# Kernel optimization log

Hardware: AMD Instinct MI355X
Metric: run time of the kernel (lower is better)

Reference implementation:

```python
import jax, jax.numpy as jnp
import numpy as np

# Hyperparameters (from init_kwargs)
D_MODEL = 1024
D_STATE = 64
HEADDIM = 64
MIMO_RANK = 2
CHUNK = 128
EXPAND = 2
D_INNER = EXPAND * D_MODEL            # 2048
NHEADS = D_INNER // HEADDIM           # 32
G = MIMO_RANK * D_STATE               # effective state channels per head = 128
D_CONV = 4
D_XBC = D_INNER + 2 * NHEADS * G      # conv channels
D_IN_PROJ = 2 * D_INNER + 2 * NHEADS * G + NHEADS  # [z, x, B, C, dt]


def rmsnorm(x, w, eps=1e-5):
    return x * w * jax.lax.rsqrt(jnp.mean(x * x, axis=-1, keepdims=True) + eps)


def setup_inputs() -> dict:
    key = jax.random.key(0)
    ks = jax.random.split(key, 8)
    B, L = 2, 2048
    x = jax.random.normal(ks[0], (B, L, D_MODEL), jnp.float32)
    norm_w = jnp.ones((D_MODEL,), jnp.float32)
    in_proj_w = jax.random.normal(ks[1], (D_IN_PROJ, D_MODEL), jnp.float32) * 0.02
    conv_w = jax.random.normal(ks[2], (D_XBC, D_CONV), jnp.float32) * 0.2
    conv_b = jnp.zeros((D_XBC,), jnp.float32)
    dt_bias = jax.random.uniform(ks[3], (NHEADS,), jnp.float32, minval=-4.0, maxval=-1.0)
    A_log = jnp.log(jax.random.uniform(ks[4], (NHEADS,), jnp.float32, minval=1.0, maxval=8.0))
    D_skip = jnp.ones((NHEADS,), jnp.float32)
    gnorm_w = jnp.ones((D_INNER,), jnp.float32)
    out_proj_w = jax.random.normal(ks[5], (D_MODEL, D_INNER), jnp.float32) * 0.02
    return dict(x=x, norm_w=norm_w, in_proj_w=in_proj_w, conv_w=conv_w, conv_b=conv_b,
                dt_bias=dt_bias, A_log=A_log, D_skip=D_skip, gnorm_w=gnorm_w,
                out_proj_w=out_proj_w)


def _mamba3(u, in_proj_w, conv_w, conv_b, dt_bias, A_log, D_skip, gnorm_w, out_proj_w):
    B, L, _ = u.shape
    H, P = NHEADS, HEADDIM
    nc = L // CHUNK

    zxbcdt = u @ in_proj_w.T                                   # (B,L,D_IN_PROJ)
    z, xbc, dt_raw = jnp.split(zxbcdt, [D_INNER, D_INNER + D_XBC], axis=-1)

    # causal depthwise conv (width D_CONV) + SiLU on [x, B, C]
    xp = jnp.pad(xbc, ((0, 0), (D_CONV - 1, 0), (0, 0)))
    conv = conv_b + sum(xp[:, k:k + L, :] * conv_w[:, k] for k in range(D_CONV))
    xbc = jax.nn.silu(conv)
    xh, Bm, Cm = jnp.split(xbc, [D_INNER, D_INNER + H * G], axis=-1)

    Xc = xh.reshape(B, nc, CHUNK, H, P)
    Bc = Bm.reshape(B, nc, CHUNK, H, G)
    Cc = Cm.reshape(B, nc, CHUNK, H, G)

    dt = jax.nn.softplus(dt_raw + dt_bias)                     # (B,L,H), positive
    A = -jnp.exp(A_log)                                        # (H,), negative
    dtc = dt.reshape(B, nc, CHUNK, H)
    a = dtc * A                                                # log decay, (B,nc,cs,H)
    cum = jnp.cumsum(a, axis=2)                                # inclusive cumsum within chunk

    # intra-chunk (quadratic, causal) part
    cumT = cum.transpose(0, 1, 3, 2)                           # (B,nc,H,cs)
    diff = cumT[..., :, None] - cumT[..., None, :]             # cum_l - cum_s
    mask = jnp.tril(jnp.ones((CHUNK, CHUNK), bool))
    decay = jnp.where(mask, jnp.exp(jnp.where(mask, diff, 0.0)), 0.0)
    dtT = dtc.transpose(0, 1, 3, 2)                            # (B,nc,H,cs)
    scores = jnp.einsum('bclhg,bcshg->bchls', Cc, Bc) * decay * dtT[:, :, :, None, :]
    Y_intra = jnp.einsum('bchls,bcshp->bclhp', scores, Xc)

    # inter-chunk state recurrence
    w = jnp.exp(cum[:, :, -1:, :] - cum) * dtc                 # (B,nc,cs,H)
    S = jnp.einsum('bcshg,bcshp->bchgp', Bc * w[..., None], Xc)  # chunk states
    dlast = jnp.exp(cum[:, :, -1, :])                          # (B,nc,H) total chunk decay

    def step(carry, inp):
        dl, s = inp
        return dl[:, :, None, None] * carry + s, carry

    init = jnp.zeros((B, H, G, P), u.dtype)
    _, Hprev = jax.lax.scan(step, init, (dlast.transpose(1, 0, 2), S.transpose(1, 0, 2, 3, 4)))
    Hprev = Hprev.transpose(1, 0, 2, 3, 4)                     # (B,nc,H,G,P) state before chunk
    Y_inter = jnp.einsum('bclhg,bchgp->bclhp', Cc * jnp.exp(cum)[..., None], Hprev)

    y = (Y_intra + Y_inter + D_skip[:, None] * Xc).reshape(B, L, D_INNER)
    y = rmsnorm(y * jax.nn.silu(z), gnorm_w)                   # gated RMSNorm
    return y @ out_proj_w.T


def reference(x, norm_w, in_proj_w, conv_w, conv_b, dt_bias, A_log, D_skip, gnorm_w, out_proj_w):
    # pre-norm residual wrapper
    return x + _mamba3(rmsnorm(x, norm_w), in_proj_w, conv_w, conv_b,
                       dt_bias, A_log, D_skip, gnorm_w, out_proj_w)
```

## Files before the change

### kernel.cpp

```cpp
#include <hip/hip_runtime.h>

typedef unsigned short u16;
typedef __attribute__((ext_vector_type(8))) short bf16x8;
typedef __attribute__((ext_vector_type(4))) float f32x4;

#define MFMA16(a,b,c) __builtin_amdgcn_mfma_f32_16x16x32_bf16(a,b,c,0,0,0)

#define DMODEL   1024
#define DINNER   2048
#define NHEADS   32
#define HEADDIM  64
#define GDIM     128
#define DXBC     10240
#define DPROJ    12320
#define CHUNK_L  128
#define NCHUNK   16
#define NROWS    4096

__device__ __forceinline__ float b2f(u16 u){ return __uint_as_float(((unsigned)u)<<16); }
__device__ __forceinline__ u16 f2b(float f){
  unsigned u = __float_as_uint(f);
  u += 0x7fffu + ((u>>16)&1u);
  return (u16)(u>>16);
}

__device__ __forceinline__ void gload_lds16(const void* g, void* l){
  __builtin_amdgcn_global_load_lds(
      (const __attribute__((address_space(1))) unsigned int*)g,
      (__attribute__((address_space(3))) unsigned int*)l, 16, 0, 0);
}

__global__ void k_f32_to_bf16(const float* __restrict__ src, u16* __restrict__ dst, int n){
  int i = blockIdx.x*blockDim.x + threadIdx.x;
  int stride = gridDim.x*blockDim.x;
  int n4 = n >> 2;
  for (int j=i; j<n4; j+=stride){
    float4 v = reinterpret_cast<const float4*>(src)[j];
    uint2 o;
    o.x = (unsigned)f2b(v.x) | ((unsigned)f2b(v.y)<<16);
    o.y = (unsigned)f2b(v.z) | ((unsigned)f2b(v.w)<<16);
    reinterpret_cast<uint2*>(dst)[j] = o;
  }
}

__global__ __launch_bounds__(256) void k_rmsnorm_in(const float* __restrict__ x,
                                                    const float* __restrict__ w,
                                                    u16* __restrict__ u){
  int row = blockIdx.x, tid = threadIdx.x;
  float4 v = reinterpret_cast<const float4*>(x + (size_t)row*DMODEL)[tid];
  float ss = v.x*v.x + v.y*v.y + v.z*v.z + v.w*v.w;
  #pragma unroll
  for (int off=32; off>0; off>>=1) ss += __shfl_down(ss, off, 64);
  __shared__ float red[4];
  if ((tid&63)==0) red[tid>>6] = ss;
  __syncthreads();
  float tot = red[0]+red[1]+red[2]+red[3];
  float sc = rsqrtf(tot/(float)DMODEL + 1e-5f);
  float4 wv = reinterpret_cast<const float4*>(w)[tid];
  uint2 o;
  o.x = (unsigned)f2b(v.x*wv.x*sc) | ((unsigned)f2b(v.y*wv.y*sc)<<16);
  o.y = (unsigned)f2b(v.z*wv.z*sc) | ((unsigned)f2b(v.w*wv.w*sc)<<16);
  reinterpret_cast<uint2*>(u + (size_t)row*DMODEL)[tid] = o;
}

__global__ __launch_bounds__(512) void k_gemm1_8p(const u16* __restrict__ A,
                                                  const u16* __restrict__ W,
                                                  u16* __restrict__ zb,
                                                  u16* __restrict__ xbc){
  __shared__ __align__(16) u16 lds[65536];
  const int tid  = threadIdx.x;
  const int lane = tid & 63, w = tid >> 6;
  const int wr = w >> 2, wc = w & 3;
  int bid = blockIdx.x;
  int xcd = bid & 7, g = bid >> 3;
  int st  = xcd*6 + (g >> 4);
  int wi  = g & 15;
  int tm  = (st/12)*4 + (wi>>2);
  int tn  = (st%12)*4 + (wi&3);
  const int m0 = tm*256, n0 = tn*256;

  const int srow = w*8 + (lane>>3);
  const int scol = ((lane&7) ^ ((lane>>3)&7))*8;
  const u16* aS = A + (size_t)(m0 + srow)*DMODEL + scol;
  const u16* bS = W + (size_t)(n0 + srow)*DMODEL + scol;
  const int ldsw = w*512;

  const int rr = lane & 15, gq = lane >> 4;

  f32x4 acc[8][4];
  #pragma unroll
  for (int i=0;i<8;i++)
    #pragma unroll
    for (int j=0;j<4;j++) acc[i][j] = (f32x4){0,0,0,0};

  auto SU_A = [&](int kt, int j){
    gload_lds16(aS + (size_t)(j*64)*DMODEL + kt*64,
                lds + (kt&1)*32768 + j*4096 + ldsw);
  };
  auto SU_B = [&](int kt, int j){
    gload_lds16(bS + (size_t)(j*64)*DMODEL + kt*64,
                lds + (kt&1)*32768 + 16384 + j*4096 + ldsw);
  };

  SU_A(0,0); SU_A(0,2); SU_B(0,0); SU_B(0,2); SU_B(0,1); SU_B(0,3); SU_A(0,1); SU_A(0,3);
  asm volatile("s_waitcnt vmcnt(2)" ::: "memory");
  __builtin_amdgcn_s_barrier();
  __builtin_amdgcn_sched_barrier(0);

  for (int kt = 0; kt < 16; ++kt){
    const u16* bufA = lds + (kt&1)*32768;
    const u16* bufB = bufA + 16384;
    const bool stg = (kt < 15);
    bf16x8 af[4][2], bw0[2][2], bw1[2][2];

    auto RDA = [&](int ti, int ks)->bf16x8{
      int r = wr*128 + ti*16 + rr;
      int s = (ks*4 + gq) ^ (rr & 7);
      return *(const bf16x8*)&bufA[r*64 + s*8];
    };
    auto RDB = [&](int tj, int ks)->bf16x8{
      int r = wc*64 + tj*16 + rr;
      int s = (ks*4 + gq) ^ (rr & 7);
      return *(const bf16x8*)&bufB[r*64 + s*8];
    };

    #pragma unroll
    for (int ti=0;ti<4;ti++){ af[ti][0]=RDA(ti,0); af[ti][1]=RDA(ti,1); }
    #pragma unroll
    for (int tj=0;tj<2;tj++){ bw0[tj][0]=RDB(tj,0); bw0[tj][1]=RDB(tj,1); }
    if (stg){ SU_A(kt+1,0); SU_A(kt+1,2); }
    __builtin_amdgcn_s_barrier();
    asm volatile("s_waitcnt lgkmcnt(0)" ::: "memory");
    __builtin_amdgcn_sched_barrier(0);
    __builtin_amdgcn_s_setprio(1);
    #pragma unroll
    for (int ti=0;ti<4;ti++)
      #pragma unroll
      for (int tj=0;tj<2;tj++){
        acc[ti][tj] = MFMA16(af[ti][0], bw0[tj][0], acc[ti][tj]);
        acc[ti][tj] = MFMA16(af[ti][1], bw0[tj][1], acc[ti][tj]);
      }
    __builtin_amdgcn_s_setprio(0);
    __builtin_amdgcn_s_barrier();

    #pragma unroll
    for (int tj=0;tj<2;tj++){ bw1[tj][0]=RDB(tj+2,0); bw1[tj][1]=RDB(tj+2,1); }
    if (stg){ SU_B(kt+1,0); SU_B(kt+1,2); }
    __builtin_amdgcn_s_barrier();
    asm volatile("s_waitcnt lgkmcnt(0)" ::: "memory");
    __builtin_amdgcn_sched_barrier(0);
    __builtin_amdgcn_s_setprio(1);
    #pragma unroll
    for (int ti=0;ti<4;ti++)
      #pragma unroll
      for (int tj=0;tj<2;tj++){
        acc[ti][tj+2] = MFMA16(af[ti][0], bw1[tj][0], acc[ti][tj+2]);
        acc[ti][tj+2] = MFMA16(af[ti][1], bw1[tj][1], acc[ti][tj+2]);
      }
    __builtin_amdgcn_s_setprio(0);
    if (stg) asm volatile("s_waitcnt vmcnt(4)" ::: "memory");
    else     asm volatile("s_waitcnt vmcnt(0)" ::: "memory");
    __builtin_amdgcn_s_barrier();

    #pragma unroll
    for (int ti=0;ti<4;ti++){ af[ti][0]=RDA(ti+4,0); af[ti][1]=RDA(ti+4,1); }
    if (stg){ SU_B(kt+1,1); SU_B(kt+1,3); }
    __builtin_amdgcn_s_barrier();
    asm volatile("s_waitcnt lgkmcnt(0)" ::: "memory");
    __builtin_amdgcn_sched_barrier(0);
    __builtin_amdgcn_s_setprio(1);
    #pragma unroll
    for (int ti=0;ti<4;ti++)
      #pragma unroll
      for (int tj=0;tj<2;tj++){
        acc[4+ti][tj] = MFMA16(af[ti][0], bw0[tj][0], acc[4+ti][tj]);
        acc[4+ti][tj] = MFMA16(af[ti][1], bw0[tj][1], acc[4+ti][tj]);
      }
    __builtin_amdgcn_s_setprio(0);
    __builtin_amdgcn_s_barrier();

    if (stg){ SU_A(kt+1,1); SU_A(kt+1,3); }
    __builtin_amdgcn_s_barrier();
    __builtin_amdgcn_sched_barrier(0);
    __builtin_amdgcn_s_setprio(1);
    #pragma unroll
    for (int ti=0;ti<4;ti++)
      #pragma unroll
      for (int tj=0;tj<2;tj++){
        acc[4+ti][tj+2] = MFMA16(af[ti][0], bw1[tj][0], acc[4+ti][tj+2]);
        acc[4+ti][tj+2] = MFMA16(af[ti][1], bw1[tj][1], acc[4+ti][tj+2]);
      }
    __builtin_amdgcn_s_setprio(0);
    if (stg){
      asm volatile("s_waitcnt vmcnt(2)" ::: "memory");
      __builtin_amdgcn_s_barrier();
      __builtin_amdgcn_sched_barrier(0);
    }
  }

  const int row0 = m0 + wr*128 + (lane>>4)*4;
  const int colb = wc*64 + (lane&15);
  if (tn >= 8){
    const int cb = n0 - DINNER;
    #pragma unroll
    for (int ti=0;ti<8;ti++)
      #pragma unroll
      for (int tj=0;tj<4;tj++)
        #pragma unroll
        for (int q=0;q<4;q++)
          xbc[(size_t)(row0 + ti*16 + q)*DXBC + cb + colb + tj*16] = f2b(acc[ti][tj][q]);
  } else {
    #pragma unroll
    for (int ti=0;ti<8;ti++)
      #pragma unroll
      for (int tj=0;tj<4;tj++)
        #pragma unroll
        for (int q=0;q<4;q++)
          zb[(size_t)(row0 + ti*16 + q)*DINNER + n0 + colb + tj*16] = f2b(acc[ti][tj][q]);
  }
}

__global__ __launch_bounds__(256) void k_gemm_dt(const u16* __restrict__ A,
                                                 const u16* __restrict__ W,
                                                 float* __restrict__ dtraw){
  const int lane = threadIdx.x & 63, wv = threadIdx.x >> 6;
  const int m0 = blockIdx.x*32;
  const int n0 = DINNER + DXBC;
  const int r  = lane & 15;
  const int kb = (lane>>4)*8;
  const int k0 = wv*256;
  const u16* a0p = A + (size_t)(m0 + r)*DMODEL + k0 + kb;
  const u16* a1p = a0p + 16*DMODEL;
  const u16* b0p = W + (size_t)(n0 + r)*DMODEL + k0 + kb;
  const u16* b1p = b0p + 16*DMODEL;
  f32x4 acc00={0,0,0,0}, acc01={0,0,0,0}, acc10={0,0,0,0}, acc11={0,0,0,0};
  #pragma unroll
  for (int k=0;k<256;k+=32){
    bf16x8 a0 = *(const bf16x8*)(a0p + k);
    bf16x8 a1 = *(const bf16x8*)(a1p + k);
    bf16x8 b0 = *(const bf16x8*)(b0p + k);
    bf16x8 b1 = *(const bf16x8*)(b1p + k);
    acc00 = MFMA16(a0,b0,acc00);
    acc01 = MFMA16(a0,b1,acc01);
    acc10 = MFMA16(a1,b0,acc10);
    acc11 = MFMA16(a1,b1,acc11);
  }
  __shared__ float part[4][1024];
  int rowb = (lane>>4)*4, col = lane&15;
  #pragma unroll
  for (int rr=0; rr<4; rr++){
    part[wv][(rowb+rr)*32 + col]         = acc00[rr];
    part[wv][(rowb+rr)*32 + col+16]      = acc01[rr];
    part[wv][(rowb+16+rr)*32 + col]      = acc10[rr];
    part[wv][(rowb+16+rr)*32 + col+16]   = acc11[rr];
  }
  __syncthreads();
  int idx = threadIdx.x*4;
  #pragma unroll
  for (int q=0;q<4;q++){
    int i = idx+q;
    dtraw[(size_t)m0*NHEADS + i] = part[0][i]+part[1][i]+part[2][i]+part[3][i];
  }
}

__global__ __launch_bounds__(256) void k_conv(const u16* __restrict__ xbc,
                                              const float* __restrict__ cw,
                                              const float* __restrict__ cb,
                                              u16* __restrict__ xh,
                                              u16* __restrict__ Bm,
                                              u16* __restrict__ Cm){
  int c  = (blockIdx.x*256 + threadIdx.x)*2;
  int row0 = blockIdx.y*8;
  int l0 = row0 & 2047;
  float4 wa = reinterpret_cast<const float4*>(cw)[c];
  float4 wb = reinterpret_cast<const float4*>(cw)[c+1];
  float cba = cb[c], cbb = cb[c+1];
  float a3=0,a2=0,a1=0, b3=0,b2=0,b1=0;
  auto loadpair = [&](int rw, float& fa, float& fb){
    unsigned v = *(const unsigned*)&xbc[(size_t)rw*DXBC + c];
    fa = b2f((u16)v); fb = b2f((u16)(v>>16));
  };
  if (l0 >= 3){
    loadpair(row0-3, a3,b3); loadpair(row0-2, a2,b2); loadpair(row0-1, a1,b1);
  }
  #pragma unroll
  for (int i=0;i<8;i++){
    float a0,b0; loadpair(row0+i, a0,b0);
    float sa = cba + a3*wa.x + a2*wa.y + a1*wa.z + a0*wa.w;
    float sb = cbb + b3*wb.x + b2*wb.y + b1*wb.z + b0*wb.w;
    sa = sa/(1.f+expf(-sa)); sb = sb/(1.f+expf(-sb));
    unsigned o = (unsigned)f2b(sa) | ((unsigned)f2b(sb)<<16);
    int rw = row0 + i;
    if (c < DINNER)            *(unsigned*)&xh[(size_t)rw*DINNER + c] = o;
    else if (c < DINNER+4096)  *(unsigned*)&Bm[(size_t)rw*4096 + (c-DINNER)] = o;
    else                       *(unsigned*)&Cm[(size_t)rw*4096 + (c-DINNER-4096)] = o;
    a3=a2; a2=a1; a1=a0; b3=b2; b2=b1; b1=b0;
  }
}

__global__ __launch_bounds__(128) void k_dtscan(const float* __restrict__ dtraw,
                                                const float* __restrict__ dt_bias,
                                                const float* __restrict__ A_log,
                                                float* __restrict__ dtT,
                                                float* __restrict__ cumT){
  int blk = blockIdx.x;
  int h   = blk & 31;
  int bc  = blk >> 5;
  int s   = threadIdx.x;
  int row = bc*128 + s;
  float xv = dtraw[(size_t)row*NHEADS + h] + dt_bias[h];
  float dt = (xv > 20.f) ? xv : log1pf(expf(xv));
  float a  = dt * (-expf(A_log[h]));
  __shared__ float lds[128];
  lds[s] = a; __syncthreads();
  #pragma unroll
  for (int off=1; off<128; off<<=1){
    float t = (s>=off) ? lds[s-off] : 0.f;
    __syncthreads();
    lds[s] += t;
    __syncthreads();
  }
  dtT[(size_t)blk*128 + s]  = dt;
  cumT[(size_t)blk*128 + s] = lds[s];
}

__global__ __launch_bounds__(256) void k_states(const u16* __restrict__ Bm,
                                                const u16* __restrict__ xh,
                                                const float* __restrict__ dtT,
                                                const float* __restrict__ cumT,
                                                float* __restrict__ S){
  int blk = blockIdx.x;
  int h = blk & 31, bc = blk >> 5;
  __shared__ __align__(16) u16 Bw[128][136];
  __shared__ __align__(16) u16 XT[64][136];
  __shared__ float cum[128], dtv[128];
  int tid = threadIdx.x;
  if (tid < 128){ cum[tid] = cumT[(size_t)blk*128+tid]; dtv[tid] = dtT[(size_t)blk*128+tid]; }
  __syncthreads();
  float clast = cum[127];
  for (int i = tid; i < 128*128; i += 256){
    int s = i >> 7, g = i & 127;
    float w = expf(clast - cum[s]) * dtv[s];
    Bw[g][s] = f2b(b2f(Bm[(size_t)(bc*128+s)*4096 + h*128 + g]) * w);
  }
  for (int i = tid; i < 64*128; i += 256){
    int s = i >> 6, p = i & 63;
    XT[p][s] = xh[(size_t)(bc*128+s)*DINNER + h*64 + p];
  }
  __syncthreads();
  int lane = tid & 63, wv = tid >> 6;
  int r = lane & 15, kb = (lane>>4)*8;
  f32x4 acc[2][4];
  #pragma unroll
  for (int i=0;i<2;i++)
    #pragma unroll
    for (int j=0;j<4;j++) acc[i][j] = (f32x4){0,0,0,0};
  #pragma unroll
  for (int k=0;k<128;k+=32){
    bf16x8 a0 = *(const bf16x8*)&Bw[wv*32 + r][k+kb];
    bf16x8 a1 = *(const bf16x8*)&Bw[wv*32 + 16 + r][k+kb];
    #pragma unroll
    for (int tj=0;tj<4;tj++){
      bf16x8 bb = *(const bf16x8*)&XT[tj*16 + r][k+kb];
      acc[0][tj] = MFMA16(a0,bb,acc[0][tj]);
      acc[1][tj] = MFMA16(a1,bb,acc[1][tj]);
    }
  }
  float* Sp = S + (size_t)blk*8192;
  int g0 = wv*32 + (lane>>4)*4, p0 = lane&15;
  #pragma unroll
  for (int ti=0;ti<2;ti++)
    #pragma unroll
    for (int tj=0;tj<4;tj++)
      #pragma unroll
      for (int rr=0;rr<4;rr++)
        Sp[(g0 + ti*16 + rr)*64 + tj*16 + p0] = acc[ti][tj][rr];
}

__global__ __launch_bounds__(256) void k_scan(const float* __restrict__ S,
                                              const float* __restrict__ cumT,
                                              u16* __restrict__ Hp){
  int slice = blockIdx.x & 7;
  int bh = blockIdx.x >> 3;
  int b = bh >> 5, h = bh & 31;
  int e0 = slice*1024 + threadIdx.x*4;
  float4 carry = {0,0,0,0};
  for (int c=0;c<NCHUNK;c++){
    int blk = (b*16+c)*32 + h;
    float dl = expf(cumT[(size_t)blk*128 + 127]);
    float4 s = *(const float4*)&S[(size_t)blk*8192 + e0];
    uint2 o;
    o.x = (unsigned)f2b(carry.x) | ((unsigned)f2b(carry.y)<<16);
    o.y = (unsigned)f2b(carry.z) | ((unsigned)f2b(carry.w)<<16);
    *reinterpret_cast<uint2*>(&Hp[(size_t)blk*8192 + e0]) = o;
    carry.x = dl*carry.x + s.x;
    carry.y = dl*carry.y + s.y;
    carry.z = dl*carry.z + s.z;
    carry.w = dl*carry.w + s.w;
  }
}

__global__ __launch_bounds__(256) void k_intra(const u16* __restrict__ Cm,
                                               const u16* __restrict__ Bm,
                                               const u16* __restrict__ xh,
                                               const u16* __restrict__ Hp,
                                               const float* __restrict__ dtT,
                                               const float* __restrict__ cumT,
                                               const float* __restrict__ Dskip,
                                               u16* __restrict__ yh){
  int blk = blockIdx.x;
  int h = blk & 31, bc = blk >> 5;
  __shared__ __align__(16) u16 Cl[128][136];
  __shared__ __align__(16) u16 Bl[128][136];
  __shared__ __align__(16) u16 XT[64][136];
  __shared__ __align__(16) u16 HT[64][136];
  __shared__ float cum[128], dtv[128];
  int tid = threadIdx.x;
  if (tid < 128){ cum[tid] = cumT[(size_t)blk*128+tid]; dtv[tid] = dtT[(size_t)blk*128+tid]; }
  for (int i = tid; i < 128*128; i += 256){
    int rw = i >> 7, g = i & 127;
    Cl[rw][g] = Cm[(size_t)(bc*128+rw)*4096 + h*128 + g];
    Bl[rw][g] = Bm[(size_t)(bc*128+rw)*4096 + h*128 + g];
  }
  for (int i = tid; i < 64*128; i += 256){
    int s = i >> 6, p = i & 63;
    XT[p][s] = xh[(size_t)(bc*128+s)*DINNER + h*64 + p];
  }
  for (int i = tid; i < 64*128; i += 256){
    int g = i >> 6, p = i & 63;
    HT[p][g] = Hp[(size_t)blk*8192 + g*64 + p];
  }
  __syncthreads();
  int lane = tid & 63, wv = tid >> 6;
  int r = lane & 15, kb = (lane>>4)*8;

  f32x4 p1[2][8];
  #pragma unroll
  for (int i=0;i<2;i++)
    #pragma unroll
    for (int j=0;j<8;j++) p1[i][j] = (f32x4){0,0,0,0};
  #pragma unroll
  for (int k=0;k<128;k+=32){
    bf16x8 a0 = *(const bf16x8*)&Cl[wv*32 + r][k+kb];
    bf16x8 a1 = *(const bf16x8*)&Cl[wv*32 + 16 + r][k+kb];
    #pragma unroll
    for (int tj=0;tj<8;tj++){
      bf16x8 bb = *(const bf16x8*)&Bl[tj*16 + r][k+kb];
      p1[0][tj] = MFMA16(a0,bb,p1[0][tj]);
      p1[1][tj] = MFMA16(a1,bb,p1[1][tj]);
    }
  }
  __syncthreads();
  int row0 = wv*32 + (lane>>4)*4;
  #pragma unroll
  for (int ti=0;ti<2;ti++)
    #pragma unroll
    for (int tj=0;tj<8;tj++)
      #pragma unroll
      for (int rr=0;rr<4;rr++){
        int l = row0 + ti*16 + rr;
        int s = tj*16 + (lane&15);
        float v = p1[ti][tj][rr];
        v = (s <= l) ? v * expf(cum[l]-cum[s]) * dtv[s] : 0.f;
        Bl[l][s] = f2b(v);
      }
  __syncthreads();

  f32x4 y[2][4];
  #pragma unroll
  for (int i=0;i<2;i++)
    #pragma unroll
    for (int j=0;j<4;j++) y[i][j] = (f32x4){0,0,0,0};
  #pragma unroll
  for (int k=0;k<128;k+=32){
    bf16x8 a0 = *(const bf16x8*)&Cl[wv*32 + r][k+kb];
    bf16x8 a1 = *(const bf16x8*)&Cl[wv*32 + 16 + r][k+kb];
    #pragma unroll
    for (int tj=0;tj<4;tj++){
      bf16x8 bb = *(const bf16x8*)&HT[tj*16 + r][k+kb];
      y[0][tj] = MFMA16(a0,bb,y[0][tj]);
      y[1][tj] = MFMA16(a1,bb,y[1][tj]);
    }
  }
  #pragma unroll
  for (int ti=0;ti<2;ti++){
    #pragma unroll
    for (int rr=0;rr<4;rr++){
      float e = expf(cum[row0 + ti*16 + rr]);
      #pragma unroll
      for (int tj=0;tj<4;tj++) y[ti][tj][rr] *= e;
    }
  }
  #pragma unroll
  for (int k=0;k<128;k+=32){
    bf16x8 a0 = *(const bf16x8*)&Bl[wv*32 + r][k+kb];
    bf16x8 a1 = *(const bf16x8*)&Bl[wv*32 + 16 + r][k+kb];
    #pragma unroll
    for (int tj=0;tj<4;tj++){
      bf16x8 bb = *(const bf16x8*)&XT[tj*16 + r][k+kb];
      y[0][tj] = MFMA16(a0,bb,y[0][tj]);
      y[1][tj] = MFMA16(a1,bb,y[1][tj]);
    }
  }
  float Dh = Dskip[h];
  #pragma unroll
  for (int ti=0;ti<2;ti++)
    #pragma unroll
    for (int tj=0;tj<4;tj++)
      #pragma unroll
      for (int rr=0;rr<4;rr++){
        int l = row0 + ti*16 + rr;
        int p = tj*16 + (lane&15);
        float xv = b2f(XT[p][l]);
        yh[(size_t)(bc*128 + l)*DINNER + h*64 + p] = f2b(y[ti][tj][rr] + Dh*xv);
      }
}

__global__ __launch_bounds__(256) void k_gate(const u16* __restrict__ yh,
                                              const u16* __restrict__ zb,
                                              const float* __restrict__ gw,
                                              u16* __restrict__ out){
  int row = blockIdx.x, tid = threadIdx.x;
  const uint4 yv = reinterpret_cast<const uint4*>(yh + (size_t)row*DINNER)[tid];
  const uint4 zv = reinterpret_cast<const uint4*>(zb + (size_t)row*DINNER)[tid];
  const unsigned* yp = (const unsigned*)&yv;
  const unsigned* zp = (const unsigned*)&zv;
  float t[8]; float ss = 0.f;
  #pragma unroll
  for (int i=0;i<4;i++){
    float y0 = b2f((u16)yp[i]), y1 = b2f((u16)(yp[i]>>16));
    float z0 = b2f((u16)zp[i]), z1 = b2f((u16)(zp[i]>>16));
    float v0 = y0 * (z0 / (1.f + expf(-z0)));
    float v1 = y1 * (z1 / (1.f + expf(-z1)));
    t[2*i] = v0; t[2*i+1] = v1; ss += v0*v0 + v1*v1;
  }
  #pragma unroll
  for (int off=32; off>0; off>>=1) ss += __shfl_down(ss, off, 64);
  __shared__ float red[4];
  if ((tid&63)==0) red[tid>>6] = ss;
  __syncthreads();
  float tot = red[0]+red[1]+red[2]+red[3];
  float g = rsqrtf(tot/(float)DINNER + 1e-5f);
  const float4 g0 = reinterpret_cast<const float4*>(gw)[tid*2];
  const float4 g1 = reinterpret_cast<const float4*>(gw)[tid*2+1];
  uint4 o;
  unsigned* op = (unsigned*)&o;
  float gg[8] = {g0.x,g0.y,g0.z,g0.w,g1.x,g1.y,g1.z,g1.w};
  #pragma unroll
  for (int i=0;i<4;i++)
    op[i] = (unsigned)f2b(t[2*i]*gg[2*i]*g) | ((unsigned)f2b(t[2*i+1]*gg[2*i+1]*g)<<16);
  reinterpret_cast<uint4*>(out + (size_t)row*DINNER)[tid] = o;
}

__global__ __launch_bounds__(256) void k_gemm2_db(const u16* __restrict__ A,
                                                  const u16* __restrict__ W,
                                                  const float* __restrict__ xres,
                                                  float* __restrict__ out){
  __shared__ __align__(16) u16 lds[2*8192];
  const int tid  = threadIdx.x;
  const int lane = tid & 63, wv = tid >> 6;
  const int wr = wv >> 1, wc = wv & 1;
  const int NWG = 8*32, Q = NWG/8;
  int swz = (blockIdx.x & 7)*Q + (blockIdx.x >> 3);
  int tm = swz / 8, tn = swz % 8;
  int m0 = tm*128, n0 = tn*128;

  const int K = DINNER;
  const int srcslot = ((lane&3) ^ ((lane>>3)&3)) * 8;
  const u16* aS0 = A + (size_t)(m0 + wv*32 + (lane>>2))*K + srcslot;
  const u16* aS1 = aS0 + (size_t)16*K;
  const u16* bS0 = W + (size_t)(n0 + wv*32 + (lane>>2))*K + srcslot;
  const u16* bS1 = bS0 + (size_t)16*K;
  const int ldsW = (wv*32)*32;
  const int rr = lane & 15;
  const int kb = (((lane>>4) ^ ((lane>>1)&3))) * 8;

  f32x4 acc[4][4];
  #pragma unroll
  for (int i=0;i<4;i++)
    #pragma unroll
    for (int j=0;j<4;j++) acc[i][j] = (f32x4){0,0,0,0};

  int stage_off = 0;
  auto STAGE = [&](int ks){
    u16* base = lds + (ks&1)*8192;
    gload_lds16(aS0 + stage_off, base + ldsW);
    gload_lds16(aS1 + stage_off, base + 16*32 + ldsW);
    gload_lds16(bS0 + stage_off, base + 4096 + ldsW);
    gload_lds16(bS1 + stage_off, base + 4096 + 16*32 + ldsW);
    stage_off += 32;
  };
  auto KSTEP = [&](int ks, int stage_ks){
    const u16* As = lds + (ks&1)*8192;
    const u16* Bs = As + 4096;
    bf16x8 af[4], bw[4];
    #pragma unroll
    for (int t=0;t<4;t++){
      af[t] = *(const bf16x8*)&As[(wr*64 + t*16 + rr)*32 + kb];
      bw[t] = *(const bf16x8*)&Bs[(wc*64 + t*16 + rr)*32 + kb];
    }
    asm volatile("s_waitcnt lgkmcnt(0)" ::: "memory");
    __builtin_amdgcn_s_barrier();
    if (stage_ks >= 0) STAGE(stage_ks);
    __builtin_amdgcn_s_setprio(1);
    #pragma unroll
    for (int ti=0;ti<4;ti++)
      #pragma unroll
      for (int tj=0;tj<4;tj++)
        acc[ti][tj] = MFMA16(af[ti], bw[tj], acc[ti][tj]);
    __builtin_amdgcn_s_setprio(0);
  };

  STAGE(0); STAGE(1);
  asm volatile("s_waitcnt vmcnt(4)" ::: "memory");
  __builtin_amdgcn_s_barrier();
  __builtin_amdgcn_sched_barrier(0);
  const int NK = K/32;
  for (int ks = 0; ks < NK-2; ++ks){
    KSTEP(ks, ks+2);
    asm volatile("s_waitcnt vmcnt(4)" ::: "memory");
    __builtin_amdgcn_s_barrier();
    __builtin_amdgcn_sched_barrier(0);
  }
  KSTEP(NK-2, -1);
  asm volatile("s_waitcnt vmcnt(0)" ::: "memory");
  __builtin_amdgcn_s_barrier();
  __builtin_amdgcn_sched_barrier(0);
  KSTEP(NK-1, -1);

  int row0 = m0 + wr*64 + (lane>>4)*4;
  int col0 = n0 + wc*64 + (lane&15);
  #pragma unroll
  for (int ti=0;ti<4;ti++)
    #pragma unroll
    for (int tj=0;tj<4;tj++)
      #pragma unroll
      for (int q=0;q<4;q++){
        size_t idx = (size_t)(row0+ti*16+q)*DMODEL + col0 + tj*16;
        out[idx] = acc[ti][tj][q] + xres[idx];
      }
}

extern "C" void kernel_launch(void* const* d_in, const int* in_sizes, int n_in,
                              void* d_out, int out_size, void* d_ws, size_t ws_size,
                              hipStream_t stream) {
  (void)in_sizes; (void)n_in; (void)out_size; (void)ws_size;
  const float* x         = (const float*)d_in[0];
  const float* norm_w    = (const float*)d_in[1];
  const float* in_proj_w = (const float*)d_in[2];
  const float* conv_w    = (const float*)d_in[3];
  const float* conv_b    = (const float*)d_in[4];
  const float* dt_bias   = (const float*)d_in[5];
  const float* A_log     = (const float*)d_in[6];
  const float* D_skip    = (const float*)d_in[7];
  const float* gnorm_w   = (const float*)d_in[8];
  const float* out_proj_w= (const float*)d_in[9];
  float* out = (float*)d_out;

  char* ws = (char*)d_ws;
  size_t off = 0;
  auto alloc = [&](size_t bytes)->char*{
    char* p = ws + off; off = (off + bytes + 255) & ~(size_t)255; return p;
  };
  u16*   W2    = (u16*)  alloc((size_t)DMODEL*DINNER*2);
  u16*   zb    = (u16*)  alloc((size_t)NROWS*DINNER*2);
  float* dtraw = (float*)alloc((size_t)NROWS*NHEADS*4);
  float* dtT   = (float*)alloc((size_t)1024*128*4);
  float* cumT  = (float*)alloc((size_t)1024*128*4);
  u16*   xhb   = (u16*)  alloc((size_t)NROWS*DINNER*2);
  u16*   Bmb   = (u16*)  alloc((size_t)NROWS*4096*2);
  u16*   Cmb   = (u16*)  alloc((size_t)NROWS*4096*2);
  char*  R1    = alloc((size_t)NROWS*DXBC*2);
  u16*   xbcr  = (u16*)R1;
  float* S     = (float*)R1;
  u16*   Hp    = (u16*)(R1 + (size_t)1024*8192*4);
  u16*   yh    = (u16*)R1;
  char*  R2    = alloc((size_t)DPROJ*DMODEL*2 + (size_t)NROWS*DMODEL*2);
  u16*   W1    = (u16*)R2;
  u16*   u_bf  = (u16*)(R2 + (size_t)DPROJ*DMODEL*2);
  u16*   gated = (u16*)R2;

  k_f32_to_bf16<<<2048,256,0,stream>>>(in_proj_w, W1, DPROJ*DMODEL);
  k_f32_to_bf16<<<512,256,0,stream>>>(out_proj_w, W2, DMODEL*DINNER);
  k_rmsnorm_in<<<NROWS,256,0,stream>>>(x, norm_w, u_bf);
  k_gemm1_8p<<<768,512,0,stream>>>(u_bf, W1, zb, xbcr);
  k_gemm_dt<<<NROWS/32,256,0,stream>>>(u_bf, W1, dtraw);
  k_conv<<<dim3(DXBC/512, NROWS/8),256,0,stream>>>(xbcr, conv_w, conv_b, xhb, Bmb, Cmb);
  k_dtscan<<<1024,128,0,stream>>>(dtraw, dt_bias, A_log, dtT, cumT);
  k_states<<<1024,256,0,stream>>>(Bmb, xhb, dtT, cumT, S);
  k_scan<<<512,256,0,stream>>>(S, cumT, Hp);
  k_intra<<<1024,256,0,stream>>>(Cmb, Bmb, xhb, Hp, dtT, cumT, D_skip, yh);
  k_gate<<<NROWS,256,0,stream>>>(yh, zb, gnorm_w, gated);
  k_gemm2_db<<<8*32,256,0,stream>>>(gated, W2, x, out);
}
```

Baseline: 317.1 us.

## Vectorize SSD chunk loads, store chunk states in bf16, skip masked intra tiles

Replaces scalar element-wise global loads in k_states and k_intra with 8- and 4-element vector loads, transposing into LDS from registers. Chunk states S are written and read as bf16 instead of fp32, which halves the traffic between k_states and k_scan, and k_scan now handles 8 elements per thread with half the grid. k_intra skips the C·B^T MFMA tiles that lie entirely above the causal diagonal, since those are masked to zero afterwards. The cost is bf16 rounding of the chunk states, which may affect accuracy, and strided LDS transpose writes that may cause bank conflicts.

```diff
diff --git a/kernel.cpp b/kernel.cpp
--- a/kernel.cpp
+++ b/kernel.cpp
@@ -328,7 +328,7 @@
                                                 const u16* __restrict__ xh,
                                                 const float* __restrict__ dtT,
                                                 const float* __restrict__ cumT,
-                                                float* __restrict__ S){
+                                                u16* __restrict__ S){
   int blk = blockIdx.x;
   int h = blk & 31, bc = blk >> 5;
   __shared__ __align__(16) u16 Bw[128][136];
@@ -338,14 +338,24 @@
   if (tid < 128){ cum[tid] = cumT[(size_t)blk*128+tid]; dtv[tid] = dtT[(size_t)blk*128+tid]; }
   __syncthreads();
   float clast = cum[127];
-  for (int i = tid; i < 128*128; i += 256){
-    int s = i >> 7, g = i & 127;
+  #pragma unroll
+  for (int it=0; it<8; ++it){
+    int s  = it*16 + (tid>>4);
+    int g8 = (tid&15)*8;
+    uint4 v = *(const uint4*)&Bm[(size_t)(bc*128+s)*4096 + h*128 + g8];
     float w = expf(clast - cum[s]) * dtv[s];
-    Bw[g][s] = f2b(b2f(Bm[(size_t)(bc*128+s)*4096 + h*128 + g]) * w);
-  }
-  for (int i = tid; i < 64*128; i += 256){
-    int s = i >> 6, p = i & 63;
-    XT[p][s] = xh[(size_t)(bc*128+s)*DINNER + h*64 + p];
+    const u16* pv = (const u16*)&v;
+    #pragma unroll
+    for (int j=0;j<8;j++) Bw[g8+j][s] = f2b(b2f(pv[j]) * w);
+  }
+  #pragma unroll
+  for (int it=0; it<8; ++it){
+    int s  = it*16 + (tid>>4);
+    int p4 = (tid&15)*4;
+    uint2 v = *(const uint2*)&xh[(size_t)(bc*128+s)*DINNER + h*64 + p4];
+    const u16* pv = (const u16*)&v;
+    #pragma unroll
+    for (int j=0;j<4;j++) XT[p4+j][s] = pv[j];
   }
   __syncthreads();
   int lane = tid & 63, wv = tid >> 6;
@@ -366,7 +376,7 @@
       acc[1][tj] = MFMA16(a1,bb,acc[1][tj]);
     }
   }
-  float* Sp = S + (size_t)blk*8192;
+  u16* Sp = S + (size_t)blk*8192;
   int g0 = wv*32 + (lane>>4)*4, p0 = lane&15;
   #pragma unroll
   for (int ti=0;ti<2;ti++)
@@ -374,29 +384,30 @@
     for (int tj=0;tj<4;tj++)
       #pragma unroll
       for (int rr=0;rr<4;rr++)
-        Sp[(g0 + ti*16 + rr)*64 + tj*16 + p0] = acc[ti][tj][rr];
-}
-
-__global__ __launch_bounds__(256) void k_scan(const float* __restrict__ S,
+        Sp[(g0 + ti*16 + rr)*64 + tj*16 + p0] = f2b(acc[ti][tj][rr]);
+}
+
+__global__ __launch_bounds__(256) void k_scan(const u16* __restrict__ S,
                                               const float* __restrict__ cumT,
                                               u16* __restrict__ Hp){
-  int slice = blockIdx.x & 7;
-  int bh = blockIdx.x >> 3;
+  int slice = blockIdx.x & 3;
+  int bh = blockIdx.x >> 2;
   int b = bh >> 5, h = bh & 31;
-  int e0 = slice*1024 + threadIdx.x*4;
-  float4 carry = {0,0,0,0};
+  int e0 = slice*2048 + threadIdx.x*8;
+  float c8[8];
+  #pragma unroll
+  for (int j=0;j<8;j++) c8[j] = 0.f;
   for (int c=0;c<NCHUNK;c++){
     int blk = (b*16+c)*32 + h;
     float dl = expf(cumT[(size_t)blk*128 + 127]);
-    float4 s = *(const float4*)&S[(size_t)blk*8192 + e0];
-    uint2 o;
-    o.x = (unsigned)f2b(carry.x) | ((unsigned)f2b(carry.y)<<16);
-    o.y = (unsigned)f2b(carry.z) | ((unsigned)f2b(carry.w)<<16);
-    *reinterpret_cast<uint2*>(&Hp[(size_t)blk*8192 + e0]) = o;
-    carry.x = dl*carry.x + s.x;
-    carry.y = dl*carry.y + s.y;
-    carry.z = dl*carry.z + s.z;
-    carry.w = dl*carry.w + s.w;
+    uint4 sv = *(const uint4*)&S[(size_t)blk*8192 + e0];
+    const u16* sp = (const u16*)&sv;
+    uint4 o; u16* op = (u16*)&o;
+    #pragma unroll
+    for (int j=0;j<8;j++) op[j] = f2b(c8[j]);
+    *reinterpret_cast<uint4*>(&Hp[(size_t)blk*8192 + e0]) = o;
+    #pragma unroll
+    for (int j=0;j<8;j++) c8[j] = dl*c8[j] + b2f(sp[j]);
   }
 }
 
@@ -417,22 +428,35 @@
   __shared__ float cum[128], dtv[128];
   int tid = threadIdx.x;
   if (tid < 128){ cum[tid] = cumT[(size_t)blk*128+tid]; dtv[tid] = dtT[(size_t)blk*128+tid]; }
-  for (int i = tid; i < 128*128; i += 256){
-    int rw = i >> 7, g = i & 127;
-    Cl[rw][g] = Cm[(size_t)(bc*128+rw)*4096 + h*128 + g];
-    Bl[rw][g] = Bm[(size_t)(bc*128+rw)*4096 + h*128 + g];
-  }
-  for (int i = tid; i < 64*128; i += 256){
-    int s = i >> 6, p = i & 63;
-    XT[p][s] = xh[(size_t)(bc*128+s)*DINNER + h*64 + p];
-  }
-  for (int i = tid; i < 64*128; i += 256){
-    int g = i >> 6, p = i & 63;
-    HT[p][g] = Hp[(size_t)blk*8192 + g*64 + p];
+  #pragma unroll
+  for (int it=0; it<8; ++it){
+    int rw = it*16 + (tid>>4);
+    int g8 = (tid&15)*8;
+    *(uint4*)&Cl[rw][g8] = *(const uint4*)&Cm[(size_t)(bc*128+rw)*4096 + h*128 + g8];
+    *(uint4*)&Bl[rw][g8] = *(const uint4*)&Bm[(size_t)(bc*128+rw)*4096 + h*128 + g8];
+  }
+  #pragma unroll
+  for (int it=0; it<8; ++it){
+    int s  = it*16 + (tid>>4);
+    int p4 = (tid&15)*4;
+    uint2 v = *(const uint2*)&xh[(size_t)(bc*128+s)*DINNER + h*64 + p4];
+    const u16* pv = (const u16*)&v;
+    #pragma unroll
+    for (int j=0;j<4;j++) XT[p4+j][s] = pv[j];
+  }
+  #pragma unroll
+  for (int it=0; it<8; ++it){
+    int g  = it*16 + (tid>>4);
+    int p4 = (tid&15)*4;
+    uint2 v = *(const uint2*)&Hp[(size_t)blk*8192 + g*64 + p4];
+    const u16* pv = (const u16*)&v;
+    #pragma unroll
+    for (int j=0;j<4;j++) HT[p4+j][g] = pv[j];
   }
   __syncthreads();
   int lane = tid & 63, wv = tid >> 6;
   int r = lane & 15, kb = (lane>>4)*8;
+  const int tjmax = 2*wv + 1;
 
   f32x4 p1[2][8];
   #pragma unroll
@@ -445,6 +469,7 @@
     bf16x8 a1 = *(const bf16x8*)&Cl[wv*32 + 16 + r][k+kb];
     #pragma unroll
     for (int tj=0;tj<8;tj++){
+      if (tj > tjmax) continue;
       bf16x8 bb = *(const bf16x8*)&Bl[tj*16 + r][k+kb];
       p1[0][tj] = MFMA16(a0,bb,p1[0][tj]);
       p1[1][tj] = MFMA16(a1,bb,p1[1][tj]);
@@ -672,7 +697,7 @@
   u16*   Cmb   = (u16*)  alloc((size_t)NROWS*4096*2);
   char*  R1    = alloc((size_t)NROWS*DXBC*2);
   u16*   xbcr  = (u16*)R1;
-  float* S     = (float*)R1;
+  u16*   S     = (u16*)R1;
   u16*   Hp    = (u16*)(R1 + (size_t)1024*8192*4);
   u16*   yh    = (u16*)R1;
   char*  R2    = alloc((size_t)DPROJ*DMODEL*2 + (size_t)NROWS*DMODEL*2);
@@ -688,7 +713,7 @@
   k_conv<<<dim3(DXBC/512, NROWS/8),256,0,stream>>>(xbcr, conv_w, conv_b, xhb, Bmb, Cmb);
   k_dtscan<<<1024,128,0,stream>>>(dtraw, dt_bias, A_log, dtT, cumT);
   k_states<<<1024,256,0,stream>>>(Bmb, xhb, dtT, cumT, S);
-  k_scan<<<512,256,0,stream>>>(S, cumT, Hp);
+  k_scan<<<256,256,0,stream>>>(S, cumT, Hp);
   k_intra<<<1024,256,0,stream>>>(Cmb, Bmb, xhb, Hp, dtT, cumT, D_skip, yh);
   k_gate<<<NROWS,256,0,stream>>>(yh, zb, gnorm_w, gated);
   k_gemm2_db<<<8*32,256,0,stream>>>(gated, W2, x, out);
```

Result: faster. 307.8 us (-2.9%).
